# Kernel optimization log

Measured on AMD Instinct MI355X. Metric: run time of the kernel, lower is better.

Reference implementation:

```python
import jax, jax.numpy as jnp
import numpy as np
import math

B, L, D_MODEL = 2, 2048, 1024
N_HEADS, D_HEAD = 16, 64
ROPE_BASE = 10000.0
PERIODS = (24, 168)
LAMBDAS = (0.5, 0.25)
NEG_INF = jnp.float32(-jnp.inf)


def _alibi_slopes(n_heads):
    # n_heads is a power of two here (16), so only the simple branch is needed
    start = 2.0 ** (-2.0 ** (-(math.log2(n_heads) - 3)))
    return jnp.asarray([start * (start ** i) for i in range(n_heads)], dtype=jnp.float32)


def _apply_rope(x, cos_t, sin_t):
    # x: [B,H,L,Dh]; cos_t/sin_t: [1,1,L,Dh//2]
    x1, x2 = x[..., 0::2], x[..., 1::2]
    xr1 = x1 * cos_t - x2 * sin_t
    xr2 = x1 * sin_t + x2 * cos_t
    return jnp.stack([xr1, xr2], axis=-1).reshape(x.shape)


def setup_inputs() -> dict:
    key = jax.random.key(0)
    ks = jax.random.split(key, 5)
    d = D_MODEL
    return {
        "x": jax.random.normal(ks[0], (B, L, d), dtype=jnp.float32),
        "Wq": jax.random.normal(ks[1], (d, d), dtype=jnp.float32) * 0.02,
        "bq": jnp.zeros((d,), dtype=jnp.float32),
        "Wk": jax.random.normal(ks[2], (d, d), dtype=jnp.float32) * 0.02,
        "bk": jnp.zeros((d,), dtype=jnp.float32),
        "Wv": jax.random.normal(ks[3], (d, d), dtype=jnp.float32) * 0.02,
        "bv": jnp.zeros((d,), dtype=jnp.float32),
        "Wo": jax.random.normal(ks[4], (d, d), dtype=jnp.float32) * 0.02,
        "bo": jnp.zeros((d,), dtype=jnp.float32),
    }


def reference(x, Wq, bq, Wk, bk, Wv, bv, Wo, bo):
    Bn, Ln, Dn = x.shape
    H, Dh = N_HEADS, D_HEAD

    def proj(W, b):
        return (x @ W + b).reshape(Bn, Ln, H, Dh).transpose(0, 2, 1, 3)  # [B,H,L,Dh]

    q, k, v = proj(Wq, bq), proj(Wk, bk), proj(Wv, bv)

    # RoPE angles: theta[l, m] = l / base^(2m/Dh)
    inv = 1.0 / (ROPE_BASE ** (jnp.arange(0, Dh, 2, dtype=jnp.float32) / Dh))
    theta = jnp.arange(Ln, dtype=jnp.float32)[:, None] * inv[None, :]  # [L, Dh/2]
    cos_t = jnp.cos(theta)[None, None]
    sin_t = jnp.sin(theta)[None, None]
    q = _apply_rope(q, cos_t, sin_t)
    k = _apply_rope(k, cos_t, sin_t)

    scale = 1.0 / math.sqrt(Dh)
    attn = jnp.einsum("bhid,bhjd->bhij", q, k) * scale  # [B,H,L,L]

    i = jnp.arange(Ln)[:, None]
    j = jnp.arange(Ln)[None, :]

    # ALiBi bias: -slope * relu(j - i), per head
    slopes = _alibi_slopes(H)  # [H]
    dist = (j - i).astype(jnp.float32)
    attn = attn + (-slopes[None, :, None, None]) * jax.nn.relu(dist)[None, None]

    # periodic cosine bias
    d_abs = jnp.abs(dist)
    pb = jnp.zeros_like(d_abs)
    for P, lam in zip(PERIODS, LAMBDAS):
        pb = pb + lam * jnp.cos(2.0 * math.pi * d_abs / float(P))
    attn = attn + pb[None, None]

    # causal mask (torch: attn + full(-inf).triu(1))
    attn = jnp.where((j > i)[None, None], NEG_INF, attn)

    p = jax.nn.softmax(attn, axis=-1)  # dropout=0 -> identity
    out = jnp.einsum("bhij,bhjd->bhid", p, v)
    out = out.transpose(0, 2, 1, 3).reshape(Bn, Ln, Dn)
    return out @ Wo + bo, p
```

## Files before the change

kernel.cpp:

```cpp
#include <hip/hip_runtime.h>
#include <math.h>

#define B_  2
#define L_  2048
#define D_  1024
#define H_  16
#define DH_ 64
#define BL_ (B_*L_)

typedef unsigned short u16;
typedef __attribute__((ext_vector_type(8))) short short8;
typedef __attribute__((ext_vector_type(4))) float f32x4;
typedef __attribute__((ext_vector_type(4))) unsigned short u16x4;

template<bool V> struct BC { static constexpr bool value = V; };

#define WS_XB   0
#define WS_WT4  2097152
#define WS_QB   4194304
#define WS_KB   6291456
#define WS_VT   8388608
#define WS_AOB  10485760
#define WS_COS  12582912
#define WS_SIN  12648448
#define WS_PBL  12713984

__device__ __forceinline__ u16 f2b(float f) {
  union { float f; unsigned u; } v; v.f = f;
  unsigned r = (v.u + 0x7fffu + ((v.u >> 16) & 1u)) >> 16;
  return (u16)r;
}
__device__ __forceinline__ u16x4 f2b4(float a, float b, float c, float d) {
  u16x4 u; u.x = f2b(a); u.y = f2b(b); u.z = f2b(c); u.w = f2b(d); return u;
}
__device__ __forceinline__ float bf2f(u16 u) {
  union { unsigned u; float f; } v; v.u = ((unsigned)u) << 16; return v.f;
}
__device__ __forceinline__ void gl_lds16(const void* g, void* l) {
  __builtin_amdgcn_global_load_lds(
      (const __attribute__((address_space(1))) unsigned int*)g,
      (__attribute__((address_space(3))) unsigned int*)l, 16, 0, 0);
}
__device__ __forceinline__ void nt_store4(float x, float y, float z, float w, float* p) {
  f32x4 v = (f32x4){x, y, z, w};
  __builtin_nontemporal_store(v, (f32x4*)p);
}

__global__ void fill_tables(float* __restrict__ costab, float* __restrict__ sintab,
                            float* __restrict__ pbl) {
  int idx = blockIdx.x * 256 + threadIdx.x;
  if (idx < L_ * 32) {
    int l = idx >> 5, tp = idx & 31;
    double inv = pow(10000.0, -2.0 * (double)tp / 64.0);
    double th  = (double)l * inv;
    costab[idx] = (float)cos(th);
    sintab[idx] = (float)sin(th);
  }
  if (idx < L_) {
    double d = (double)idx;
    double v = 0.5  * cos(6.283185307179586 * d / 24.0)
             + 0.25 * cos(6.283185307179586 * d / 168.0);
    pbl[idx] = (float)(v * 1.4426950408889634);
  }
}

__global__ __launch_bounds__(256) void xcast(const float* __restrict__ x, u16* __restrict__ xb) {
  const size_t i = ((size_t)blockIdx.x * 256 + threadIdx.x) * 8;
  float4 a = *(const float4*)(x + i);
  float4 b = *(const float4*)(x + i + 4);
  u16 us[8] = { f2b(a.x),f2b(a.y),f2b(a.z),f2b(a.w), f2b(b.x),f2b(b.y),f2b(b.z),f2b(b.w) };
  *(short8*)(xb + i) = *(short8*)us;
}

__global__ __launch_bounds__(256) void wtrans4(const float* __restrict__ W0, const float* __restrict__ W1,
                                               const float* __restrict__ W2, const float* __restrict__ W3,
                                               u16* __restrict__ Wt) {
  __shared__ u16 tt[64][80];
  const int z = blockIdx.z;
  const float* W = (z == 0) ? W0 : (z == 1) ? W1 : (z == 2) ? W2 : W3;
  u16* Wtz = Wt + (size_t)z * 1024 * 1024;
  const int k0 = blockIdx.x << 6, n0 = blockIdx.y << 6;
  const int t = threadIdx.x;
  {
    const int r = t >> 4, c4 = (t & 15) << 2;
    for (int rr = r; rr < 64; rr += 16) {
      float4 v = *(const float4*)(W + (size_t)(k0 + rr) * D_ + n0 + c4);
      tt[c4+0][rr] = f2b(v.x); tt[c4+1][rr] = f2b(v.y);
      tt[c4+2][rr] = f2b(v.z); tt[c4+3][rr] = f2b(v.w);
    }
  }
  __syncthreads();
  const int n = t >> 2, kc = (t & 3) << 4;
  u16* dst = Wtz + (size_t)(n0 + n) * D_ + k0 + kc;
  #pragma unroll
  for (int u = 0; u < 16; ++u) dst[u] = tt[n][kc + u];
}

template<int KIND>
__global__ __launch_bounds__(256) void gemm_k(
    const u16* __restrict__ Ag, const u16* __restrict__ Bg,
    const float* __restrict__ b0, const float* __restrict__ b1, const float* __restrict__ b2,
    const float* __restrict__ costab, const float* __restrict__ sintab,
    u16* __restrict__ O0, u16* __restrict__ O1, u16* __restrict__ O2,
    float* __restrict__ Cout)
{
  __shared__ u16 As[8192];
  __shared__ u16 Bs[8192];
  const int t = threadIdx.x, w = t >> 6, lane = t & 63;
  const int lt = lane & 15, lg = lane >> 4;
  const int wg = blockIdx.x + (blockIdx.y << 5);
  int sid;
  if constexpr (KIND == 1) sid = (wg & 7) * 96 + (wg >> 3);
  else                     sid = (wg & 7) * 32 + (wg >> 3);
  const int row0 = (sid & 31) << 7;
  const int gy   = sid >> 5;
  const int col0 = gy << 7;
  const int wm = (w & 1) << 6, wn = (w >> 1) << 6;
  const int proj = (KIND == 1) ? (gy >> 3) : 0;
  const bool swp = (KIND == 0) || (proj < 2);

  const int srow = lane >> 3;
  const int gch  = (lane & 7) ^ (srow & 7);
  const u16* aptr[4]; const u16* bptr[4];
  char* adst[4]; char* bdst[4];
  #pragma unroll
  for (int u = 0; u < 4; ++u) {
    const int rl = w * 32 + u * 8 + srow;
    aptr[u] = Ag + (size_t)(row0 + rl) * 1024 + gch * 8;
    bptr[u] = Bg + (size_t)(col0 + rl) * 1024 + gch * 8;
    adst[u] = (char*)As + (w * 32 + u * 8) * 128;
    bdst[u] = (char*)Bs + (w * 32 + u * 8) * 128;
  }
  int aoff[2][4], boff[2][4];
  #pragma unroll
  for (int ks = 0; ks < 2; ++ks)
    #pragma unroll
    for (int q = 0; q < 4; ++q) {
      const int ra = wm + q * 16 + lt;
      aoff[ks][q] = ra * 128 + (((ks * 4 + lg) ^ (ra & 7)) << 4);
      const int rb = wn + q * 16 + lt;
      boff[ks][q] = rb * 128 + (((ks * 4 + lg) ^ (rb & 7)) << 4);
    }

  f32x4 acc[4][4];
  #pragma unroll
  for (int i = 0; i < 4; ++i)
    #pragma unroll
    for (int j = 0; j < 4; ++j) acc[i][j] = (f32x4){0.f,0.f,0.f,0.f};

  auto loop = [&](auto SW) {
    for (int kt = 0; kt < 16; ++kt) {
      #pragma unroll
      for (int u = 0; u < 4; ++u) {
        gl_lds16(aptr[u] + kt * 64, adst[u]);
        gl_lds16(bptr[u] + kt * 64, bdst[u]);
      }
      __syncthreads();
      #pragma unroll
      for (int ks = 0; ks < 2; ++ks) {
        short8 af[4], bf[4];
        #pragma unroll
        for (int q = 0; q < 4; ++q) {
          af[q] = *(const short8*)((const char*)As + aoff[ks][q]);
          bf[q] = *(const short8*)((const char*)Bs + boff[ks][q]);
        }
        #pragma unroll
        for (int mi = 0; mi < 4; ++mi)
          #pragma unroll
          for (int nj = 0; nj < 4; ++nj) {
            if constexpr (decltype(SW)::value)
              acc[mi][nj] = __builtin_amdgcn_mfma_f32_16x16x32_bf16(bf[nj], af[mi], acc[mi][nj], 0, 0, 0);
            else
              acc[mi][nj] = __builtin_amdgcn_mfma_f32_16x16x32_bf16(af[mi], bf[nj], acc[mi][nj], 0, 0, 0);
          }
      }
      __syncthreads();
    }
  };
  if (swp) loop(BC<true>{}); else loop(BC<false>{});

  if constexpr (KIND == 0) {
    #pragma unroll
    for (int mi = 0; mi < 4; ++mi) {
      const int m = row0 + wm + mi * 16 + lt;
      #pragma unroll
      for (int nj = 0; nj < 4; ++nj) {
        const int nb = col0 + wn + nj * 16 + (lg << 2);
        float4 bb = *(const float4*)(b0 + nb);
        nt_store4(acc[mi][nj][0] + bb.x, acc[mi][nj][1] + bb.y,
                  acc[mi][nj][2] + bb.z, acc[mi][nj][3] + bb.w,
                  Cout + (size_t)m * 1024 + nb);
      }
    }
  } else if (proj < 2) {
    const float* bias = proj ? b1 : b0;
    u16* Ob = proj ? O1 : O0;
    const int col0p = (gy & 7) << 7;
    #pragma unroll
    for (int mi = 0; mi < 4; ++mi) {
      const int m = row0 + wm + mi * 16 + lt;
      const int bb_ = m >> 11, lpos = m & (L_ - 1);
      #pragma unroll
      for (int nj = 0; nj < 4; ++nj) {
        const int nb = col0p + wn + nj * 16 + (lg << 2);
        const int d0 = nb & 63, h = nb >> 6;
        float4 ba = *(const float4*)(bias + nb);
        const float o0 = acc[mi][nj][0] + ba.x, o1 = acc[mi][nj][1] + ba.y;
        const float o2 = acc[mi][nj][2] + ba.z, o3 = acc[mi][nj][3] + ba.w;
        const float* ct = costab + lpos * 32 + (d0 >> 1);
        const float* st = sintab + lpos * 32 + (d0 >> 1);
        const float c0 = ct[0], c1 = ct[1], s0 = st[0], s1 = st[1];
        const float r0 = o0 * c0 - o1 * s0, r1 = o0 * s0 + o1 * c0;
        const float r2 = o2 * c1 - o3 * s1, r3 = o2 * s1 + o3 * c1;
        *(u16x4*)(Ob + ((size_t)(bb_ * 16 + h) * L_ + lpos) * 64 + d0) = f2b4(r0, r1, r2, r3);
      }
    }
  } else {
    const int col0p = (gy & 7) << 7;
    #pragma unroll
    for (int mi = 0; mi < 4; ++mi) {
      const int lb = row0 + wm + mi * 16 + (lg << 2);
      const int bb_ = lb >> 11;
      #pragma unroll
      for (int nj = 0; nj < 4; ++nj) {
        const int n = col0p + wn + nj * 16 + lt;
        const int h = n >> 6, dh = n & 63;
        const float bv1 = b2[n];
        *(u16x4*)(O2 + ((size_t)(bb_ * 16 + h) * 64 + dh) * L_ + (lb & (L_ - 1))) =
            f2b4(acc[mi][nj][0] + bv1, acc[mi][nj][1] + bv1,
                 acc[mi][nj][2] + bv1, acc[mi][nj][3] + bv1);
      }
    }
  }
}

__global__ __launch_bounds__(512, 4) void attn_mfma(
    const u16* __restrict__ Qb, const u16* __restrict__ Kb, const u16* __restrict__ Vt,
    const float* __restrict__ pbg, float* __restrict__ Pout, u16* __restrict__ AOb)
{
  __shared__ u16 PL[33 * 16 * 64];
  __shared__ float PVacc[2][16][64];
  __shared__ float lsbuf[8][2][16];
  float* pbl = &PVacc[0][0][0];
  const int t = threadIdx.x, w = t >> 6, lane = t & 63;
  const int lt = lane & 15, lg = lane >> 4;
  *(float4*)(pbl + t * 4) = *(const float4*)(pbg + t * 4);
  const int wg = blockIdx.x + (blockIdx.y << 6);
  const int sid = (wg & 7) * 256 + (wg >> 3);
  const int bh = sid >> 6, pr = sid & 63;
  const int b = bh >> 4, h = bh & 15;
  const int sA = pr, sB = 127 - pr;
  const int kvA = (sA >> 2) + 1, kvB = (sB >> 2) + 1;
  const int swz = (lt & 7) << 4;
  const float C1 = 0.18033688011112042f;
  char* PLb = (char*)PL;
  __syncthreads();

  f32x4 oaccA[4], oaccB[4];
  #pragma unroll
  for (int dt = 0; dt < 4; ++dt) {
    oaccA[dt] = (f32x4){0.f,0.f,0.f,0.f};
    oaccB[dt] = (f32x4){0.f,0.f,0.f,0.f};
  }
  float lsumA = 0.f, lsumB = 0.f;

  auto tile = [&](int s, int kvt, const short8& q0, const short8& q1,
                  f32x4* oacc, float& lsum, int pb0, int rstride, bool masked) {
    const int j0 = kvt << 6;
    const int i  = s * 16 + lt;
    const u16* kp = Kb + ((size_t)bh * L_ + j0 + lt) * 64 + lg * 8;
    short8 kf[8];
    #pragma unroll
    for (int jt = 0; jt < 4; ++jt) {
      kf[2*jt]   = *(const short8*)(kp + jt * 1024);
      kf[2*jt+1] = *(const short8*)(kp + jt * 1024 + 32);
    }
    f32x4 z[4];
    #pragma unroll
    for (int jt = 0; jt < 4; ++jt) {
      f32x4 zz = (f32x4){0.f,0.f,0.f,0.f};
      zz = __builtin_amdgcn_mfma_f32_16x16x32_bf16(kf[2*jt],   q0, zz, 0, 0, 0);
      zz = __builtin_amdgcn_mfma_f32_16x16x32_bf16(kf[2*jt+1], q1, zz, 0, 0, 0);
      z[jt] = zz;
    }
    const u16* vp = Vt + ((size_t)bh * 64 + lt) * L_ + j0 + lg * 8;
    short8 vf[8];
    #pragma unroll
    for (int dt = 0; dt < 4; ++dt) {
      vf[2*dt]   = *(const short8*)(vp + dt * 16 * L_);
      vf[2*dt+1] = *(const short8*)(vp + dt * 16 * L_ + 32);
    }
    #pragma unroll
    for (int jt = 0; jt < 4; ++jt) {
      const int jb = j0 + jt * 16 + (lg << 2);
      const int dd = i - jb;
      float pr4[4];
      if (masked) {
        #pragma unroll
        for (int r = 0; r < 4; ++r) {
          const int d  = dd - r;
          const int dc = d < 0 ? 0 : d;
          const float pe = exp2f(fmaf(z[jt][r], C1, pbl[dc]));
          pr4[r] = d < 0 ? 0.f : pe;
          lsum += pr4[r];
        }
      } else {
        #pragma unroll
        for (int r = 0; r < 4; ++r) {
          pr4[r] = exp2f(fmaf(z[jt][r], C1, pbl[dd - r]));
          lsum += pr4[r];
        }
      }
      *(u16x4*)(PLb + pb0 + lt * rstride + ((kvt * 128 + jt * 32 + lg * 8) ^ swz)) =
          f2b4(pr4[0], pr4[1], pr4[2], pr4[3]);
    }
    short8 pa0 = *(const short8*)(PLb + pb0 + lt * rstride + ((kvt * 128 + lg * 16) ^ swz));
    short8 pa1 = *(const short8*)(PLb + pb0 + lt * rstride + ((kvt * 128 + 64 + lg * 16) ^ swz));
    #pragma unroll
    for (int dt = 0; dt < 4; ++dt) {
      oacc[dt] = __builtin_amdgcn_mfma_f32_16x16x32_bf16(pa0, vf[2*dt],   oacc[dt], 0, 0, 0);
      oacc[dt] = __builtin_amdgcn_mfma_f32_16x16x32_bf16(pa1, vf[2*dt+1], oacc[dt], 0, 0, 0);
    }
  };

  {
    const u16* qpA = Qb + ((size_t)bh * L_ + sA * 16 + lt) * 64 + lg * 8;
    const short8 qA0 = *(const short8*)(qpA), qA1 = *(const short8*)(qpA + 32);
    for (int kvt = w; kvt < kvA; kvt += 8)
      tile(sA, kvt, qA0, qA1, oaccA, lsumA, 0, kvA << 7, kvt == kvA - 1);
  }
  {
    const u16* qpB = Qb + ((size_t)bh * L_ + sB * 16 + lt) * 64 + lg * 8;
    const short8 qB0 = *(const short8*)(qpB), qB1 = *(const short8*)(qpB + 32);
    const int st0 = (8 + w - (kvA & 7)) & 7;
    for (int kvt = st0; kvt < kvB; kvt += 8)
      tile(sB, kvt, qB0, qB1, oaccB, lsumB, kvA << 11, kvB << 7, kvt == kvB - 1);
  }

  lsumA += __shfl_xor(lsumA, 16); lsumA += __shfl_xor(lsumA, 32);
  lsumB += __shfl_xor(lsumB, 16); lsumB += __shfl_xor(lsumB, 32);
  if (lane < 16) { lsbuf[w][0][lt] = lsumA; lsbuf[w][1][lt] = lsumB; }
  __syncthreads();

  #pragma unroll
  for (int rp = 0; rp < 4; ++rp) {
    const int rid = rp * 8 + w;
    const int st = rid >> 4, rl = rid & 15;
    const int s_ = st ? sB : sA;
    const int i  = s_ * 16 + rl;
    float den = 0.f;
    #pragma unroll
    for (int ww = 0; ww < 8; ++ww) den += lsbuf[ww][st][rl];
    const float rv = 1.f / den;
    const char* rb = PLb + (st ? (kvA << 11) : 0) + rl * ((st ? kvB : kvA) << 7);
    const int rsw = (rl & 7) << 4;
    float* prow = Pout + ((size_t)bh * L_ + i) * L_;
    const int lim4 = i >> 2;
    #pragma unroll
    for (int cc = 0; cc < 8; ++cc) {
      const int c4 = lane + cc * 64;
      float ox = 0.f, oy = 0.f, oz = 0.f, ow = 0.f;
      if (c4 <= lim4) {
        u16x4 dv = *(const u16x4*)(rb + ((c4 << 3) ^ rsw));
        ox = bf2f(dv.x) * rv; oy = bf2f(dv.y) * rv;
        oz = bf2f(dv.z) * rv; ow = bf2f(dv.w) * rv;
        if (c4 == lim4) {
          const int j0c = c4 << 2;
          if (j0c + 1 > i) oy = 0.f;
          if (j0c + 2 > i) oz = 0.f;
          if (j0c + 3 > i) ow = 0.f;
        }
      }
      nt_store4(ox, oy, oz, ow, prow + (c4 << 2));
    }
  }

  for (int rr = 0; rr < 8; ++rr) {
    if (w == rr) {
      #pragma unroll
      for (int dt = 0; dt < 4; ++dt)
        #pragma unroll
        for (int r = 0; r < 4; ++r) {
          if (rr == 0) {
            PVacc[0][(lg << 2) + r][dt * 16 + lt] = oaccA[dt][r];
            PVacc[1][(lg << 2) + r][dt * 16 + lt] = oaccB[dt][r];
          } else {
            PVacc[0][(lg << 2) + r][dt * 16 + lt] += oaccA[dt][r];
            PVacc[1][(lg << 2) + r][dt * 16 + lt] += oaccB[dt][r];
          }
        }
    }
    __syncthreads();
  }

  {
    const int st = t >> 8, rl = (t >> 4) & 15, c0 = (t & 15) << 2;
    float den = 0.f;
    #pragma unroll
    for (int ww = 0; ww < 8; ++ww) den += lsbuf[ww][st][rl];
    const float rv = 1.f / den;
    const int s_ = st ? sB : sA;
    const int i = s_ * 16 + rl;
    u16x4 o = f2b4(PVacc[st][rl][c0] * rv, PVacc[st][rl][c0 + 1] * rv,
                   PVacc[st][rl][c0 + 2] * rv, PVacc[st][rl][c0 + 3] * rv);
    *(u16x4*)(AOb + ((size_t)(b * L_ + i)) * 1024 + h * 64 + c0) = o;
  }
}

extern "C" void kernel_launch(void* const* d_in, const int* in_sizes, int n_in,
                              void* d_out, int out_size, void* d_ws, size_t ws_size,
                              hipStream_t stream) {
  const float* x  = (const float*)d_in[0];
  const float* Wq = (const float*)d_in[1];
  const float* bq = (const float*)d_in[2];
  const float* Wk = (const float*)d_in[3];
  const float* bk = (const float*)d_in[4];
  const float* Wv = (const float*)d_in[5];
  const float* bv = (const float*)d_in[6];
  const float* Wo = (const float*)d_in[7];
  const float* bo = (const float*)d_in[8];

  float* out  = (float*)d_out;
  float* Pout = out + (size_t)BL_ * D_;

  float* ws = (float*)d_ws;
  u16* XB  = (u16*)(ws + WS_XB);
  u16* WT4 = (u16*)(ws + WS_WT4);
  u16* QB  = (u16*)(ws + WS_QB);
  u16* KB  = (u16*)(ws + WS_KB);
  u16* VT  = (u16*)(ws + WS_VT);
  u16* AOB = (u16*)(ws + WS_AOB);
  float* cosT = ws + WS_COS;
  float* sinT = ws + WS_SIN;
  float* pblG = ws + WS_PBL;

  fill_tables<<<256, 256, 0, stream>>>(cosT, sinT, pblG);
  xcast<<<2048, 256, 0, stream>>>(x, XB);
  wtrans4<<<dim3(16,16,4), 256, 0, stream>>>(Wq, Wk, Wv, Wo, WT4);

  gemm_k<1><<<dim3(32,24), 256, 0, stream>>>(XB, WT4, bq, bk, bv, cosT, sinT,
                                             QB, KB, VT, nullptr);

  attn_mfma<<<dim3(64,32), 512, 0, stream>>>(QB, KB, VT, pblG, Pout, AOB);

  gemm_k<0><<<dim3(32,8), 256, 0, stream>>>(AOB, WT4 + (size_t)3*1024*1024, bo,
                                            nullptr, nullptr, nullptr, nullptr,
                                            nullptr, nullptr, nullptr, out);
}
```

Measured before the change: 256.9 us.

## Overlap strip-A probability stores with strip-B attention compute

```diff
diff --git a/kernel.cpp b/kernel.cpp
--- a/kernel.cpp
+++ b/kernel.cpp
@@ -329,49 +329,147 @@
     for (int kvt = w; kvt < kvA; kvt += 8)
       tile(sA, kvt, qA0, qA1, oaccA, lsumA, 0, kvA << 7, kvt == kvA - 1);
   }
+  lsumA += __shfl_xor(lsumA, 16); lsumA += __shfl_xor(lsumA, 32);
+  if (lane < 16) lsbuf[w][0][lt] = lsumA;
+  __syncthreads();
+
+  float rvA[2]; const char* rbA[2]; float* prowA[2]; int limA[2], rswA[2];
+  #pragma unroll
+  for (int u = 0; u < 2; ++u) {
+    const int rl = w * 2 + u;
+    float den = 0.f;
+    #pragma unroll
+    for (int ww = 0; ww < 8; ++ww) den += lsbuf[ww][0][rl];
+    rvA[u] = 1.f / den;
+    rbA[u] = PLb + rl * (kvA << 7);
+    rswA[u] = (rl & 7) << 4;
+    const int i = sA * 16 + rl;
+    limA[u] = i >> 2;
+    prowA[u] = Pout + ((size_t)bh * L_ + i) * L_;
+  }
+  int chunk = 0;
+  auto storeA = [&](int c) {
+    const int u = c >> 3, cc = c & 7;
+    const int c4 = lane + cc * 64;
+    float ox = 0.f, oy = 0.f, oz = 0.f, ow = 0.f;
+    if (c4 <= limA[u]) {
+      u16x4 dv = *(const u16x4*)(rbA[u] + ((c4 << 3) ^ rswA[u]));
+      const float rv = rvA[u];
+      ox = bf2f(dv.x) * rv; oy = bf2f(dv.y) * rv;
+      oz = bf2f(dv.z) * rv; ow = bf2f(dv.w) * rv;
+      if (c4 == limA[u]) {
+        const int i = sA * 16 + (w * 2 + u);
+        const int j0c = c4 << 2;
+        if (j0c + 1 > i) oy = 0.f;
+        if (j0c + 2 > i) oz = 0.f;
+        if (j0c + 3 > i) ow = 0.f;
+      }
+    }
+    nt_store4(ox, oy, oz, ow, prowA[u] + (c4 << 2));
+  };
+
   {
     const u16* qpB = Qb + ((size_t)bh * L_ + sB * 16 + lt) * 64 + lg * 8;
     const short8 qB0 = *(const short8*)(qpB), qB1 = *(const short8*)(qpB + 32);
-    const int st0 = (8 + w - (kvA & 7)) & 7;
-    for (int kvt = st0; kvt < kvB; kvt += 8)
-      tile(sB, kvt, qB0, qB1, oaccB, lsumB, kvA << 11, kvB << 7, kvt == kvB - 1);
-  }
-
-  lsumA += __shfl_xor(lsumA, 16); lsumA += __shfl_xor(lsumA, 32);
+    const int pb0 = kvA << 11, rstride = kvB << 7;
+    const int iB = sB * 16 + lt;
+    for (int kvt = w; kvt < kvB; kvt += 8) {
+      const bool masked = (kvt == kvB - 1);
+      const int j0 = kvt << 6;
+      const u16* kp = Kb + ((size_t)bh * L_ + j0 + lt) * 64 + lg * 8;
+      short8 kf[8];
+      #pragma unroll
+      for (int jt = 0; jt < 4; ++jt) {
+        kf[2*jt]   = *(const short8*)(kp + jt * 1024);
+        kf[2*jt+1] = *(const short8*)(kp + jt * 1024 + 32);
+      }
+      f32x4 z[4];
+      #pragma unroll
+      for (int jt = 0; jt < 4; ++jt) {
+        f32x4 zz = (f32x4){0.f,0.f,0.f,0.f};
+        zz = __builtin_amdgcn_mfma_f32_16x16x32_bf16(kf[2*jt],   qB0, zz, 0, 0, 0);
+        zz = __builtin_amdgcn_mfma_f32_16x16x32_bf16(kf[2*jt+1], qB1, zz, 0, 0, 0);
+        z[jt] = zz;
+      }
+      const u16* vp = Vt + ((size_t)bh * 64 + lt) * L_ + j0 + lg * 8;
+      short8 vf[8];
+      #pragma unroll
+      for (int dt = 0; dt < 4; ++dt) {
+        vf[2*dt]   = *(const short8*)(vp + dt * 16 * L_);
+        vf[2*dt+1] = *(const short8*)(vp + dt * 16 * L_ + 32);
+      }
+      {
+        const int lim = (chunk + 6 < 16) ? chunk + 6 : 16;
+        for (; chunk < lim; ++chunk) storeA(chunk);
+      }
+      #pragma unroll
+      for (int jt = 0; jt < 4; ++jt) {
+        const int jb = j0 + jt * 16 + (lg << 2);
+        const int dd = iB - jb;
+        float pr4[4];
+        if (masked) {
+          #pragma unroll
+          for (int r = 0; r < 4; ++r) {
+            const int d  = dd - r;
+            const int dc = d < 0 ? 0 : d;
+            const float pe = exp2f(fmaf(z[jt][r], C1, pbl[dc]));
+            pr4[r] = d < 0 ? 0.f : pe;
+            lsumB += pr4[r];
+          }
+        } else {
+          #pragma unroll
+          for (int r = 0; r < 4; ++r) {
+            pr4[r] = exp2f(fmaf(z[jt][r], C1, pbl[dd - r]));
+            lsumB += pr4[r];
+          }
+        }
+        *(u16x4*)(PLb + pb0 + lt * rstride + ((kvt * 128 + jt * 32 + lg * 8) ^ swz)) =
+            f2b4(pr4[0], pr4[1], pr4[2], pr4[3]);
+      }
+      short8 pa0 = *(const short8*)(PLb + pb0 + lt * rstride + ((kvt * 128 + lg * 16) ^ swz));
+      short8 pa1 = *(const short8*)(PLb + pb0 + lt * rstride + ((kvt * 128 + 64 + lg * 16) ^ swz));
+      #pragma unroll
+      for (int dt = 0; dt < 4; ++dt) {
+        oaccB[dt] = __builtin_amdgcn_mfma_f32_16x16x32_bf16(pa0, vf[2*dt],   oaccB[dt], 0, 0, 0);
+        oaccB[dt] = __builtin_amdgcn_mfma_f32_16x16x32_bf16(pa1, vf[2*dt+1], oaccB[dt], 0, 0, 0);
+      }
+    }
+    for (; chunk < 16; ++chunk) storeA(chunk);
+  }
+
   lsumB += __shfl_xor(lsumB, 16); lsumB += __shfl_xor(lsumB, 32);
-  if (lane < 16) { lsbuf[w][0][lt] = lsumA; lsbuf[w][1][lt] = lsumB; }
+  if (lane < 16) lsbuf[w][1][lt] = lsumB;
   __syncthreads();
-
-  #pragma unroll
-  for (int rp = 0; rp < 4; ++rp) {
-    const int rid = rp * 8 + w;
-    const int st = rid >> 4, rl = rid & 15;
-    const int s_ = st ? sB : sA;
-    const int i  = s_ * 16 + rl;
-    float den = 0.f;
-    #pragma unroll
-    for (int ww = 0; ww < 8; ++ww) den += lsbuf[ww][st][rl];
-    const float rv = 1.f / den;
-    const char* rb = PLb + (st ? (kvA << 11) : 0) + rl * ((st ? kvB : kvA) << 7);
-    const int rsw = (rl & 7) << 4;
-    float* prow = Pout + ((size_t)bh * L_ + i) * L_;
-    const int lim4 = i >> 2;
-    #pragma unroll
-    for (int cc = 0; cc < 8; ++cc) {
-      const int c4 = lane + cc * 64;
-      float ox = 0.f, oy = 0.f, oz = 0.f, ow = 0.f;
-      if (c4 <= lim4) {
-        u16x4 dv = *(const u16x4*)(rb + ((c4 << 3) ^ rsw));
-        ox = bf2f(dv.x) * rv; oy = bf2f(dv.y) * rv;
-        oz = bf2f(dv.z) * rv; ow = bf2f(dv.w) * rv;
-        if (c4 == lim4) {
-          const int j0c = c4 << 2;
-          if (j0c + 1 > i) oy = 0.f;
-          if (j0c + 2 > i) oz = 0.f;
-          if (j0c + 3 > i) ow = 0.f;
+  {
+    #pragma unroll
+    for (int u = 0; u < 2; ++u) {
+      const int rl = w * 2 + u;
+      float den = 0.f;
+      #pragma unroll
+      for (int ww = 0; ww < 8; ++ww) den += lsbuf[ww][1][rl];
+      const float rv = 1.f / den;
+      const char* rb = PLb + (kvA << 11) + rl * (kvB << 7);
+      const int rsw = (rl & 7) << 4;
+      const int i = sB * 16 + rl;
+      float* prow = Pout + ((size_t)bh * L_ + i) * L_;
+      const int lim4 = i >> 2;
+      #pragma unroll
+      for (int cc = 0; cc < 8; ++cc) {
+        const int c4 = lane + cc * 64;
+        float ox = 0.f, oy = 0.f, oz = 0.f, ow = 0.f;
+        if (c4 <= lim4) {
+          u16x4 dv = *(const u16x4*)(rb + ((c4 << 3) ^ rsw));
+          ox = bf2f(dv.x) * rv; oy = bf2f(dv.y) * rv;
+          oz = bf2f(dv.z) * rv; ow = bf2f(dv.w) * rv;
+          if (c4 == lim4) {
+            const int j0c = c4 << 2;
+            if (j0c + 1 > i) oy = 0.f;
+            if (j0c + 2 > i) oz = 0.f;
+            if (j0c + 3 > i) ow = 0.f;
+          }
         }
-      }
-      nt_store4(ox, oy, oz, ow, prow + (c4 << 2));
+        nt_store4(ox, oy, oz, ow, prow + (c4 << 2));
+      }
     }
   }
 
@@ -392,7 +490,6 @@
     }
     __syncthreads();
   }
-
   {
     const int st = t >> 8, rl = (t >> 4) & 15, c0 = (t & 15) << 2;
     float den = 0.f;
```

After: 292.7 us. +13.9%, slower.
